# Kernel tuning notes

Hardware: AMD Instinct MI355X
Metric: run time of the kernel (lower is better)

## Reference

```python
import jax, jax.numpy as jnp
import numpy as np

B, H, W, C, NH = 400, 14, 14, 768, 12
HD = C // NH  # 64


def setup_inputs() -> dict:
    key = jax.random.key(0)
    ks = jax.random.split(key, 6)
    s = 0.02
    return {
        "hidden_states": jax.random.normal(ks[0], (B, H, W, C), jnp.float32),
        "qkv_w": jax.random.normal(ks[1], (3 * C, C), jnp.float32) * s,
        "qkv_b": jnp.zeros((3 * C,), jnp.float32),
        "proj_w": jax.random.normal(ks[2], (C, C), jnp.float32) * s,
        "proj_b": jnp.zeros((C,), jnp.float32),
        "rel_pos_h": jax.random.normal(ks[3], (2 * H - 1, HD), jnp.float32) * s,
        "rel_pos_w": jax.random.normal(ks[4], (2 * W - 1, HD), jnp.float32) * s,
    }


def _get_rel_pos(q_size, k_size, rel_pos):
    # q_size == k_size and table already has 2*k-1 entries -> pure gather,
    # matching SamVisionAttention.get_rel_pos without interpolation.
    coords = jnp.arange(q_size)[:, None] - jnp.arange(k_size)[None, :] + (k_size - 1)
    return rel_pos[coords]  # (q, k, head_dim)


def reference(hidden_states, qkv_w, qkv_b, proj_w, proj_b, rel_pos_h, rel_pos_w):
    b, h, w, c = hidden_states.shape
    scale = HD ** -0.5
    # qkv projection: (b, h*w, 3c) -> (3, b, nh, hw, hd)
    qkv = hidden_states.reshape(b, h * w, c) @ qkv_w.T + qkv_b
    qkv = qkv.reshape(b, h * w, 3, NH, HD).transpose(2, 0, 3, 1, 4)
    q, k, v = qkv[0], qkv[1], qkv[2]
    # decomposed relative position bias (computed from UNSCALED q, as in SAM)
    Rh = _get_rel_pos(h, h, rel_pos_h)  # (h, h, hd)
    Rw = _get_rel_pos(w, w, rel_pos_w)  # (w, w, hd)
    qr = q.reshape(b, NH, h, w, HD)
    rel_h = jnp.einsum('bnhwc,hkc->bnhwk', qr, Rh)  # (b, nh, h, w, h)
    rel_w = jnp.einsum('bnhwc,wkc->bnhwk', qr, Rw)  # (b, nh, h, w, w)
    bias = (rel_h[..., :, None] + rel_w[..., None, :]).reshape(b, NH, h * w, h * w)
    # attention
    attn = jnp.einsum('bnqd,bnkd->bnqk', q, k) * scale + bias
    attn = jax.nn.softmax(attn, axis=-1)
    out = jnp.einsum('bnqk,bnkd->bnqd', attn, v)
    out = out.transpose(0, 2, 1, 3).reshape(b, h, w, c)
    return out @ proj_w.T + proj_b
```

## Files before the change

### kernel.cpp

```cpp
#include <hip/hip_runtime.h>
#include <hip/hip_bf16.h>

typedef __bf16 bfv8 __attribute__((ext_vector_type(8)));
typedef float f32x4 __attribute__((ext_vector_type(4)));
typedef unsigned short u16;
typedef unsigned int u32;

#define MT 78400

#define SBAR() __builtin_amdgcn_s_barrier()
#define VMCNT(n) asm volatile("s_waitcnt vmcnt(" #n ")" ::: "memory")

__device__ __forceinline__ u16 f2bf(float f) {
  u32 x = __float_as_uint(f);
  return (u16)((x + 0x7FFFu + ((x >> 16) & 1u)) >> 16);
}

__device__ __forceinline__ void gld16(const void* g, void* l) {
  __builtin_amdgcn_global_load_lds((const __attribute__((address_space(1))) void*)g,
                                   (__attribute__((address_space(3))) void*)l, 16, 0, 0);
}

__global__ __launch_bounds__(256) void cvt_f32_bf16(const float* __restrict__ src,
                                                    u16* __restrict__ dst, int n8) {
  int stride = gridDim.x * 256;
  for (int i = blockIdx.x * 256 + threadIdx.x; i < n8; i += stride) {
    const float4* s = (const float4*)(src + (long)i * 8);
    float4 a = s[0], b = s[1];
    u32 p0 = f2bf(a.x) | ((u32)f2bf(a.y) << 16);
    u32 p1 = f2bf(a.z) | ((u32)f2bf(a.w) << 16);
    u32 p2 = f2bf(b.x) | ((u32)f2bf(b.y) << 16);
    u32 p3 = f2bf(b.z) | ((u32)f2bf(b.w) << 16);
    uint4 o = {p0, p1, p2, p3};
    *(uint4*)(dst + (long)i * 8) = o;
  }
}


__device__ __forceinline__ void stageA(const u16* __restrict__ A, u16* SH, int sl,
                                       int m0, int kt, int h, int tid) {
#pragma unroll
  for (int i = 0; i < 2; ++i) {
    int c = tid + 512 * i;
    int r = c >> 3, s = c & 7;
    int gc = s ^ (r & 7);
    int mr = m0 + h * 128 + r; if (mr > MT - 1) mr = MT - 1;
    gld16(A + mr * 768 + kt * 64 + gc * 8, SH + sl * 32768 + h * 8192 + c * 8);
  }
}

__device__ __forceinline__ void stageB(const u16* __restrict__ W, u16* SH, int sl,
                                       int n0, int kt, int h, int tid) {
#pragma unroll
  for (int i = 0; i < 2; ++i) {
    int c = tid + 512 * i;
    int r = c >> 3, s = c & 7;
    int gc = s ^ (r & 7);
    gld16(W + (n0 + h * 128 + r) * 768 + kt * 64 + gc * 8,
          SH + sl * 32768 + 16384 + h * 8192 + c * 8);
  }
}

__device__ __forceinline__ void gemm256_main(const u16* __restrict__ A, const u16* __restrict__ W,
                                             u16* SH, int m0, int n0, int tid,
                                             f32x4 (&acc)[8][4]) {
  const int lane = tid & 63;
  const int q15 = lane & 15, g = lane >> 4;
  const int wid = tid >> 6;
  const int wm = wid >> 2, wn = wid & 3;
  const int q7 = q15 & 7;
  const int x0 = (g ^ q7) << 3;
  const int arow0 = wm * 128 + q15;
  const int brow0 = wn * 64 + q15;

  stageB(W, SH, 0, n0, 0, 0, tid); stageB(W, SH, 0, n0, 0, 1, tid);
  stageA(A, SH, 0, m0, 0, 0, tid); stageA(A, SH, 0, m0, 0, 1, tid);
  stageB(W, SH, 1, n0, 1, 0, tid); stageB(W, SH, 1, n0, 1, 1, tid);
  VMCNT(4);
  SBAR();

  for (int u = 0; u < 12; ++u) {
    const int sl = u & 1;
    const u16* Sa = SH + sl * 32768;
    const u16* Sb = Sa + 16384;
    const int ka = (u + 1 < 12) ? u + 1 : 11;
    const int kb = (u + 2 < 12) ? u + 2 : 11;
    bfv8 b0[4], b1[4];
#pragma unroll
    for (int p = 0; p < 4; ++p) {
      if (p == 0) {
#pragma unroll
        for (int ni = 0; ni < 4; ++ni) {
          const u16* bp = Sb + (brow0 + ni * 16) * 64;
          b0[ni] = *(const bfv8*)(bp + x0);
          b1[ni] = *(const bfv8*)(bp + (x0 ^ 32));
        }
      }
      bfv8 a0[2], a1[2];
#pragma unroll
      for (int m2 = 0; m2 < 2; ++m2) {
        const u16* ap = Sa + (arow0 + (p * 2 + m2) * 16) * 64;
        a0[m2] = *(const bfv8*)(ap + x0);
        a1[m2] = *(const bfv8*)(ap + (x0 ^ 32));
      }
      if (p == 0)      stageA(A, SH, sl ^ 1, m0, ka, 0, tid);
      else if (p == 1) stageA(A, SH, sl ^ 1, m0, ka, 1, tid);
      else if (p == 2) stageB(W, SH, sl, n0, kb, 0, tid);
      else           { stageB(W, SH, sl, n0, kb, 1, tid); VMCNT(4); }
      SBAR();
      __builtin_amdgcn_s_setprio(1);
#pragma unroll
      for (int m2 = 0; m2 < 2; ++m2)
#pragma unroll
        for (int ni = 0; ni < 4; ++ni)
          acc[p * 2 + m2][ni] = __builtin_amdgcn_mfma_f32_16x16x32_bf16(a0[m2], b0[ni], acc[p * 2 + m2][ni], 0, 0, 0);
#pragma unroll
      for (int m2 = 0; m2 < 2; ++m2)
#pragma unroll
        for (int ni = 0; ni < 4; ++ni)
          acc[p * 2 + m2][ni] = __builtin_amdgcn_mfma_f32_16x16x32_bf16(a1[m2], b1[ni], acc[p * 2 + m2][ni], 0, 0, 0);
      __builtin_amdgcn_s_setprio(0);
      SBAR();
    }
  }
}

__global__ __launch_bounds__(512, 2) void qkv_gemm(const u16* __restrict__ A, const u16* __restrict__ W,
                                                   const float* __restrict__ bias,
                                                   u16* __restrict__ Qo, u16* __restrict__ Ko,
                                                   u16* __restrict__ Vo) {
  extern __shared__ u16 SH[];
  const int tid = threadIdx.x;
  const int orig = blockIdx.x;
  const int xcd = orig & 7, ii = orig >> 3;
  const int wg = (xcd < 3 ? xcd * 346 : 1038 + (xcd - 3) * 345) + ii;
  const int mt = wg / 9, nt = wg - mt * 9;
  const int m0 = mt * 256, n0 = nt * 256;

  f32x4 acc[8][4];
#pragma unroll
  for (int i = 0; i < 8; ++i)
#pragma unroll
    for (int j = 0; j < 4; ++j) acc[i][j] = (f32x4){0.f, 0.f, 0.f, 0.f};

  gemm256_main(A, W, SH, m0, n0, tid, acc);

  const int lane = tid & 63, q15 = lane & 15, g = lane >> 4;
  const int wid = tid >> 6, wm = wid >> 2, wn = wid & 3;
  __syncthreads();
  const int sel = nt / 3;
  u16* dst = (sel == 0) ? Qo : (sel == 1) ? Ko : Vo;
  const int ntr = nt - sel * 3;
  u16* Cs = SH;

#pragma unroll
  for (int h = 0; h < 2; ++h) {
    if (wm == h) {
#pragma unroll
      for (int ni = 0; ni < 4; ++ni) {
        int col = wn * 64 + ni * 16 + q15;
        float bb = bias[n0 + col];
#pragma unroll
        for (int mi = 0; mi < 8; ++mi)
#pragma unroll
          for (int r = 0; r < 4; ++r)
            Cs[(mi * 16 + g * 4 + r) * 264 + col] = f2bf(acc[mi][ni][r] + bb);
      }
    }
    __syncthreads();
#pragma unroll
    for (int j = 0; j < 8; ++j) {
      int idx = tid + 512 * j;
      int row = idx >> 5, cc = idx & 31;
      int m = m0 + h * 128 + row;
      if (m < MT) {
        int b = m / 196, s = m - b * 196;
        int nh = ntr * 4 + (cc >> 3);
        int hd0 = (cc & 7) * 8;
        uint4 v = *(const uint4*)(Cs + row * 264 + cc * 8);
        *(uint4*)(dst + (long)b * 150528 + (long)s * 64 + nh * 12544 + hd0) = v;
      }
    }
    if (h == 0) __syncthreads();
  }
}

__global__ __launch_bounds__(512, 2) void proj_gemm(const u16* __restrict__ A, const u16* __restrict__ W,
                                                    const float* __restrict__ bias,
                                                    float* __restrict__ out) {
  extern __shared__ u16 SH[];
  const int tid = threadIdx.x;
  const int orig = blockIdx.x;
  const int xcd = orig & 7, ii = orig >> 3;
  const int wg = (xcd < 1 ? xcd * 116 : 116 + (xcd - 1) * 115) + ii;
  const int mt = wg / 3, nt = wg - mt * 3;
  const int m0 = mt * 256, n0 = nt * 256;

  f32x4 acc[8][4];
#pragma unroll
  for (int i = 0; i < 8; ++i)
#pragma unroll
    for (int j = 0; j < 4; ++j) acc[i][j] = (f32x4){0.f, 0.f, 0.f, 0.f};

  gemm256_main(A, W, SH, m0, n0, tid, acc);

  const int lane = tid & 63, q15 = lane & 15, g = lane >> 4;
  const int wid = tid >> 6, wm = wid >> 2, wn = wid & 3;

#pragma unroll
  for (int ni = 0; ni < 4; ++ni) {
    int n = n0 + wn * 64 + ni * 16 + q15;
    float bb = bias[n];
#pragma unroll
    for (int mi = 0; mi < 8; ++mi)
#pragma unroll
      for (int r = 0; r < 4; ++r) {
        int m = m0 + wm * 128 + mi * 16 + g * 4 + r;
        if (m < MT) out[(long)m * 768 + n] = acc[mi][ni][r] + bb;
      }
  }
}

#define KLDS_OFF 0
#define INDK_OFF 29952
#define VT_OFF   46592
#define TH_OFF   79360
#define TW_OFF   83248
#define AW_OFF   87136
#define P_OFF    97376
#define SMEM_SZ  156768

__global__ __launch_bounds__(512, 2) void attn_kernel(const u16* __restrict__ Q, const u16* __restrict__ K,
                                                      const u16* __restrict__ V,
                                                      const float* __restrict__ rph, const float* __restrict__ rpw,
                                                      u16* __restrict__ AO) {
  extern __shared__ char smem[];
  u16* Klds = (u16*)(smem + KLDS_OFF);
  u16* IndK = (u16*)(smem + INDK_OFF);
  u16* VT = (u16*)(smem + VT_OFF);
  u16* TH = (u16*)(smem + TH_OFF);
  u16* TW = (u16*)(smem + TW_OFF);
  const int tid = threadIdx.x, lane = tid & 63, wid = tid >> 6;
  const int q15 = lane & 15, g = lane >> 4;
  const int bnh = blockIdx.x;
  const int b = bnh / 12, nh = bnh - b * 12;
  const u16* Qg = Q + bnh * 12544;
  const u16* Kg = K + bnh * 12544;
  const u16* Vg = V + bnh * 12544;
  u16* Pw = (u16*)(smem + P_OFF) + wid * 16 * 232;
  u16* AWw = (u16*)(smem + AW_OFF) + wid * 16 * 40;

  for (int c = tid; c < 1764; c += 512) {
    int krow = c / 9, part = c - krow * 9;
    gld16(Kg + krow * 64 + part * 8, Klds + c * 8);
  }
  for (int i = tid; i < 208 * 40; i += 512) {
    int k = i / 40, j = i - (i / 40) * 40;
    int hk = k / 14, wk = k - hk * 14;
    IndK[i] = (j == hk || j == 16 + wk) ? 0x3F80 : 0;
  }
  for (int idx = tid; idx < 1792; idx += 512) {
    int k = idx >> 3, nb = idx & 7;
    u32 w0 = 0, w1 = 0, w2 = 0, w3 = 0;
    if (k < 196) {
      uint4 t = *(const uint4*)(Vg + k * 64 + nb * 8);
      w0 = t.x; w1 = t.y; w2 = t.z; w3 = t.w;
    }
    u32 wv[4] = {w0, w1, w2, w3};
#pragma unroll
    for (int j = 0; j < 8; j++) {
      int n = nb * 8 + j;
      u16 val = (u16)(wv[j >> 1] >> ((j & 1) * 16));
      int blk = (k >> 3) ^ (n & 7) ^ (n >> 3);
      VT[n * 256 + blk * 8 + (k & 7)] = val;
    }
  }
  for (int i = tid; i < 27 * 64; i += 512) {
    int r = i >> 6, cc = i & 63;
    TH[r * 72 + cc] = f2bf(rph[i]);
    TW[r * 72 + cc] = f2bf(rpw[i]);
  }
  for (int i = lane; i < 16 * 24; i += 64) Pw[(i / 24) * 232 + 208 + (i % 24)] = 0;
  __syncthreads();

  const f32x4 zero = {0.f, 0.f, 0.f, 0.f};
  for (int qt = wid; qt < 13; qt += 8) {
    const int q0 = qt * 16;
    int qrow = q0 + q15; if (qrow > 195) qrow = 195;
    bfv8 qf0 = *(const bfv8*)(Qg + qrow * 64 + g * 8);
    bfv8 qf1 = *(const bfv8*)(Qg + qrow * 64 + 32 + g * 8);

    int hq0 = q0 / 14, hq1 = (q0 + 15) / 14;
    int rha = hq0 + 13 - q15; rha = rha < 0 ? 0 : (rha > 26 ? 26 : rha);
    int rhb = hq1 + 13 - q15; rhb = rhb < 0 ? 0 : (rhb > 26 ? 26 : rhb);
    int rwa = q15;
    int rwb = 16 + q15; if (rwb > 26) rwb = 26;
    f32x4 c0h = zero, c1h = zero, c0w = zero, c1w = zero;
    {
      bfv8 t0 = *(const bfv8*)(TH + rha * 72 + g * 8);
      bfv8 t1 = *(const bfv8*)(TH + rha * 72 + 32 + g * 8);
      c0h = __builtin_amdgcn_mfma_f32_16x16x32_bf16(qf0, t0, c0h, 0, 0, 0);
      c0h = __builtin_amdgcn_mfma_f32_16x16x32_bf16(qf1, t1, c0h, 0, 0, 0);
      bfv8 t2 = *(const bfv8*)(TH + rhb * 72 + g * 8);
      bfv8 t3 = *(const bfv8*)(TH + rhb * 72 + 32 + g * 8);
      c1h = __builtin_amdgcn_mfma_f32_16x16x32_bf16(qf0, t2, c1h, 0, 0, 0);
      c1h = __builtin_amdgcn_mfma_f32_16x16x32_bf16(qf1, t3, c1h, 0, 0, 0);
      bfv8 u0 = *(const bfv8*)(TW + rwa * 72 + g * 8);
      bfv8 u1 = *(const bfv8*)(TW + rwa * 72 + 32 + g * 8);
      c0w = __builtin_amdgcn_mfma_f32_16x16x32_bf16(qf0, u0, c0w, 0, 0, 0);
      c0w = __builtin_amdgcn_mfma_f32_16x16x32_bf16(qf1, u1, c0w, 0, 0, 0);
      bfv8 u2 = *(const bfv8*)(TW + rwb * 72 + g * 8);
      bfv8 u3 = *(const bfv8*)(TW + rwb * 72 + 32 + g * 8);
      c1w = __builtin_amdgcn_mfma_f32_16x16x32_bf16(qf0, u2, c1w, 0, 0, 0);
      c1w = __builtin_amdgcn_mfma_f32_16x16x32_bf16(qf1, u3, c1w, 0, 0, 0);
    }

#pragma unroll
    for (int r = 0; r < 4; r++) {
      int row = g * 4 + r;
      int qq = q0 + row;
      int hqr = qq / 14;
      int wq_r = qq - hqr * 14;
      if (q15 < 10) AWw[row * 40 + 30 + q15] = 0;
      float rh = ((hqr == hq1) ? c1h[r] : c0h[r]) * 8.0f;
      AWw[row * 40 + q15] = (q15 <= 13) ? f2bf(rh) : (u16)0;
      int w0p = wq_r + 13 - q15;
      if (w0p >= 0 && w0p <= 13) AWw[row * 40 + 16 + w0p] = f2bf(c0w[r] * 8.0f);
      int w1p = wq_r - 3 - q15;
      if (w1p >= 0 && w1p <= 13) AWw[row * 40 + 16 + w1p] = f2bf(c1w[r] * 8.0f);
    }
    bfv8 qaug = *(const bfv8*)(AWw + q15 * 40 + g * 8);

    float den[4] = {0.f, 0.f, 0.f, 0.f};
#pragma unroll
    for (int t = 0; t < 13; t++) {
      bfv8 kb0 = *(const bfv8*)(Klds + (t * 16 + q15) * 72 + g * 8);
      bfv8 kb1 = *(const bfv8*)(Klds + (t * 16 + q15) * 72 + 32 + g * 8);
      bfv8 ib = *(const bfv8*)(IndK + (t * 16 + q15) * 40 + g * 8);
      __builtin_amdgcn_s_setprio(1);
      f32x4 a0 = __builtin_amdgcn_mfma_f32_16x16x32_bf16(qaug, ib, zero, 0, 0, 0);
      f32x4 a1 = __builtin_amdgcn_mfma_f32_16x16x32_bf16(qf0, kb0, a0, 0, 0, 0);
      f32x4 st = __builtin_amdgcn_mfma_f32_16x16x32_bf16(qf1, kb1, a1, 0, 0, 0);
      __builtin_amdgcn_s_setprio(0);
#pragma unroll
      for (int r = 0; r < 4; r++) {
        float v = st[r] * 0.125f - 4.0f;
        float p = (t == 12 && q15 >= 4) ? 0.f : exp2f(v * 1.44269504f);
        den[r] += p;
        Pw[(g * 4 + r) * 232 + t * 16 + q15] = f2bf(p);
      }
    }
#pragma unroll
    for (int r = 0; r < 4; r++) {
      den[r] += __shfl_xor(den[r], 1);
      den[r] += __shfl_xor(den[r], 2);
      den[r] += __shfl_xor(den[r], 4);
      den[r] += __shfl_xor(den[r], 8);
    }

    f32x4 o[4] = {zero, zero, zero, zero};
    __builtin_amdgcn_s_setprio(1);
#pragma unroll
    for (int ks = 0; ks < 7; ks++) {
      bfv8 pa = *(const bfv8*)(Pw + q15 * 232 + ks * 32 + g * 8);
#pragma unroll
      for (int nt = 0; nt < 4; nt++) {
        int n = nt * 16 + q15;
        int blk = ((ks * 4 + g) ^ (n & 7) ^ (n >> 3));
        bfv8 vb = *(const bfv8*)(VT + n * 256 + blk * 8);
        o[nt] = __builtin_amdgcn_mfma_f32_16x16x32_bf16(pa, vb, o[nt], 0, 0, 0);
      }
    }
    __builtin_amdgcn_s_setprio(0);

    float inv[4];
#pragma unroll
    for (int r = 0; r < 4; r++) inv[r] = 1.0f / den[r];
#pragma unroll
    for (int nt = 0; nt < 4; nt++)
#pragma unroll
      for (int r = 0; r < 4; r++) {
        int s_ = q0 + g * 4 + r;
        if (s_ < 196) AO[((long)(b * 196 + s_)) * 768 + nh * 64 + nt * 16 + q15] = f2bf(o[nt][r] * inv[r]);
      }
  }
}

#define GEMM_LDS 131072

extern "C" void kernel_launch(void* const* d_in, const int* in_sizes, int n_in,
                              void* d_out, int out_size, void* d_ws, size_t ws_size,
                              hipStream_t stream) {
  const float* hs = (const float*)d_in[0];
  const float* qkvw = (const float*)d_in[1];
  const float* qkvb = (const float*)d_in[2];
  const float* projw = (const float*)d_in[3];
  const float* projb = (const float*)d_in[4];
  const float* rph = (const float*)d_in[5];
  const float* rpw = (const float*)d_in[6];

  char* ws = (char*)d_ws;
  u16* Xb = (u16*)ws;
  u16* Wq = (u16*)(ws + 120422400);
  u16* Wp = (u16*)(ws + 123961344);
  u16* Qb = (u16*)(ws + 125140992);
  u16* Kb = (u16*)(ws + 245563392);
  u16* Vb = (u16*)(ws + 365985792);
  u16* AO = Xb;

  cvt_f32_bf16<<<2048, 256, 0, stream>>>(hs, Xb, 7526400);
  cvt_f32_bf16<<<864, 256, 0, stream>>>(qkvw, Wq, 221184);
  cvt_f32_bf16<<<288, 256, 0, stream>>>(projw, Wp, 73728);

  hipFuncSetAttribute((const void*)qkv_gemm, hipFuncAttributeMaxDynamicSharedMemorySize, GEMM_LDS);
  qkv_gemm<<<2763, 512, GEMM_LDS, stream>>>(Xb, Wq, qkvb, Qb, Kb, Vb);

  hipFuncSetAttribute((const void*)attn_kernel, hipFuncAttributeMaxDynamicSharedMemorySize, SMEM_SZ);
  attn_kernel<<<4800, 512, SMEM_SZ, stream>>>(Qb, Kb, Vb, rph, rpw, AO);

  hipFuncSetAttribute((const void*)proj_gemm, hipFuncAttributeMaxDynamicSharedMemorySize, GEMM_LDS);
  proj_gemm<<<921, 512, GEMM_LDS, stream>>>(AO, Wp, projb, (float*)d_out);
}
```

Before: 866.8 us.

## Software-pipeline GEMM LDS fragment loads and swizzle K tile in attention

Restructures the GEMM main loop so the A/B fragment reads for the next sub-step are issued from LDS right after a barrier and overlap the MFMAs of the current step. The B fragments and first A fragments for the next k-tile are prefetched at the end of each iteration, and the staging order is rearranged to match. In the attention kernel, the padded K tile in LDS (stride 72) is replaced with an XOR-swizzled stride-64 layout, which shrinks shared memory and avoids bank conflicts. The scale and log2e constants in the softmax exponent are folded into one fused multiply-add. The new schedule adds register pressure and depends on the reordered barriers and vmcnt waits being correct.

```diff
diff --git a/kernel.cpp b/kernel.cpp
--- a/kernel.cpp
+++ b/kernel.cpp
@@ -68,61 +68,137 @@
   const int q15 = lane & 15, g = lane >> 4;
   const int wid = tid >> 6;
   const int wm = wid >> 2, wn = wid & 3;
-  const int q7 = q15 & 7;
-  const int x0 = (g ^ q7) << 3;
+  const int x0 = (g ^ (q15 & 7)) << 3;
   const int arow0 = wm * 128 + q15;
   const int brow0 = wn * 64 + q15;
+
+  bfv8 b0[4], b1[4];
+  bfv8 aX0[2], aX1[2], aY0[2], aY1[2];
 
   stageB(W, SH, 0, n0, 0, 0, tid); stageB(W, SH, 0, n0, 0, 1, tid);
   stageA(A, SH, 0, m0, 0, 0, tid); stageA(A, SH, 0, m0, 0, 1, tid);
   stageB(W, SH, 1, n0, 1, 0, tid); stageB(W, SH, 1, n0, 1, 1, tid);
+  stageA(A, SH, 1, m0, 1, 0, tid);
   VMCNT(4);
   SBAR();
+  {
+    const u16* Sb = SH + 16384;
+#pragma unroll
+    for (int ni = 0; ni < 4; ++ni) {
+      const u16* bp = Sb + (brow0 + ni * 16) * 64;
+      b0[ni] = *(const bfv8*)(bp + x0);
+      b1[ni] = *(const bfv8*)(bp + (x0 ^ 32));
+    }
+#pragma unroll
+    for (int m2 = 0; m2 < 2; ++m2) {
+      const u16* ap = SH + (arow0 + m2 * 16) * 64;
+      aX0[m2] = *(const bfv8*)(ap + x0);
+      aX1[m2] = *(const bfv8*)(ap + (x0 ^ 32));
+    }
+  }
 
   for (int u = 0; u < 12; ++u) {
     const int sl = u & 1;
     const u16* Sa = SH + sl * 32768;
-    const u16* Sb = Sa + 16384;
-    const int ka = (u + 1 < 12) ? u + 1 : 11;
-    const int kb = (u + 2 < 12) ? u + 2 : 11;
-    bfv8 b0[4], b1[4];
-#pragma unroll
-    for (int p = 0; p < 4; ++p) {
-      if (p == 0) {
-#pragma unroll
-        for (int ni = 0; ni < 4; ++ni) {
-          const u16* bp = Sb + (brow0 + ni * 16) * 64;
-          b0[ni] = *(const bfv8*)(bp + x0);
-          b1[ni] = *(const bfv8*)(bp + (x0 ^ 32));
-        }
-      }
-      bfv8 a0[2], a1[2];
+    const u16* San = SH + (sl ^ 1) * 32768;
+    const u16* Sbn = San + 16384;
+    const int kn1 = (u + 1 < 12) ? u + 1 : 11;
+    const int kn2 = (u + 2 < 12) ? u + 2 : 11;
+
+    __builtin_amdgcn_s_setprio(1);
+#pragma unroll
+    for (int m2 = 0; m2 < 2; ++m2)
+#pragma unroll
+      for (int ni = 0; ni < 4; ++ni)
+        acc[m2][ni] = __builtin_amdgcn_mfma_f32_16x16x32_bf16(aX0[m2], b0[ni], acc[m2][ni], 0, 0, 0);
+#pragma unroll
+    for (int m2 = 0; m2 < 2; ++m2)
+#pragma unroll
+      for (int ni = 0; ni < 4; ++ni)
+        acc[m2][ni] = __builtin_amdgcn_mfma_f32_16x16x32_bf16(aX1[m2], b1[ni], acc[m2][ni], 0, 0, 0);
+    __builtin_amdgcn_s_setprio(0);
+    SBAR();
+#pragma unroll
+    for (int m2 = 0; m2 < 2; ++m2) {
+      const u16* ap = Sa + (arow0 + (2 + m2) * 16) * 64;
+      aY0[m2] = *(const bfv8*)(ap + x0);
+      aY1[m2] = *(const bfv8*)(ap + (x0 ^ 32));
+    }
+    stageA(A, SH, sl ^ 1, m0, kn1, 1, tid);
+
+    __builtin_amdgcn_s_setprio(1);
+#pragma unroll
+    for (int m2 = 0; m2 < 2; ++m2)
+#pragma unroll
+      for (int ni = 0; ni < 4; ++ni)
+        acc[2 + m2][ni] = __builtin_amdgcn_mfma_f32_16x16x32_bf16(aY0[m2], b0[ni], acc[2 + m2][ni], 0, 0, 0);
+#pragma unroll
+    for (int m2 = 0; m2 < 2; ++m2)
+#pragma unroll
+      for (int ni = 0; ni < 4; ++ni)
+        acc[2 + m2][ni] = __builtin_amdgcn_mfma_f32_16x16x32_bf16(aY1[m2], b1[ni], acc[2 + m2][ni], 0, 0, 0);
+    __builtin_amdgcn_s_setprio(0);
+    SBAR();
+#pragma unroll
+    for (int m2 = 0; m2 < 2; ++m2) {
+      const u16* ap = Sa + (arow0 + (4 + m2) * 16) * 64;
+      aX0[m2] = *(const bfv8*)(ap + x0);
+      aX1[m2] = *(const bfv8*)(ap + (x0 ^ 32));
+    }
+    stageB(W, SH, sl, n0, kn2, 0, tid);
+
+    __builtin_amdgcn_s_setprio(1);
+#pragma unroll
+    for (int m2 = 0; m2 < 2; ++m2)
+#pragma unroll
+      for (int ni = 0; ni < 4; ++ni)
+        acc[4 + m2][ni] = __builtin_amdgcn_mfma_f32_16x16x32_bf16(aX0[m2], b0[ni], acc[4 + m2][ni], 0, 0, 0);
+#pragma unroll
+    for (int m2 = 0; m2 < 2; ++m2)
+#pragma unroll
+      for (int ni = 0; ni < 4; ++ni)
+        acc[4 + m2][ni] = __builtin_amdgcn_mfma_f32_16x16x32_bf16(aX1[m2], b1[ni], acc[4 + m2][ni], 0, 0, 0);
+    __builtin_amdgcn_s_setprio(0);
+    SBAR();
+#pragma unroll
+    for (int m2 = 0; m2 < 2; ++m2) {
+      const u16* ap = Sa + (arow0 + (6 + m2) * 16) * 64;
+      aY0[m2] = *(const bfv8*)(ap + x0);
+      aY1[m2] = *(const bfv8*)(ap + (x0 ^ 32));
+    }
+    stageB(W, SH, sl, n0, kn2, 1, tid);
+
+    __builtin_amdgcn_s_setprio(1);
+#pragma unroll
+    for (int m2 = 0; m2 < 2; ++m2)
+#pragma unroll
+      for (int ni = 0; ni < 4; ++ni)
+        acc[6 + m2][ni] = __builtin_amdgcn_mfma_f32_16x16x32_bf16(aY0[m2], b0[ni], acc[6 + m2][ni], 0, 0, 0);
+#pragma unroll
+    for (int m2 = 0; m2 < 2; ++m2)
+#pragma unroll
+      for (int ni = 0; ni < 4; ++ni)
+        acc[6 + m2][ni] = __builtin_amdgcn_mfma_f32_16x16x32_bf16(aY1[m2], b1[ni], acc[6 + m2][ni], 0, 0, 0);
+    __builtin_amdgcn_s_setprio(0);
+    VMCNT(4);
+    SBAR();
+    if (u < 11) {
+#pragma unroll
+      for (int ni = 0; ni < 4; ++ni) {
+        const u16* bp = Sbn + (brow0 + ni * 16) * 64;
+        b0[ni] = *(const bfv8*)(bp + x0);
+        b1[ni] = *(const bfv8*)(bp + (x0 ^ 32));
+      }
 #pragma unroll
       for (int m2 = 0; m2 < 2; ++m2) {
-        const u16* ap = Sa + (arow0 + (p * 2 + m2) * 16) * 64;
-        a0[m2] = *(const bfv8*)(ap + x0);
-        a1[m2] = *(const bfv8*)(ap + (x0 ^ 32));
-      }
-      if (p == 0)      stageA(A, SH, sl ^ 1, m0, ka, 0, tid);
-      else if (p == 1) stageA(A, SH, sl ^ 1, m0, ka, 1, tid);
-      else if (p == 2) stageB(W, SH, sl, n0, kb, 0, tid);
-      else           { stageB(W, SH, sl, n0, kb, 1, tid); VMCNT(4); }
-      SBAR();
-      __builtin_amdgcn_s_setprio(1);
-#pragma unroll
-      for (int m2 = 0; m2 < 2; ++m2)
-#pragma unroll
-        for (int ni = 0; ni < 4; ++ni)
-          acc[p * 2 + m2][ni] = __builtin_amdgcn_mfma_f32_16x16x32_bf16(a0[m2], b0[ni], acc[p * 2 + m2][ni], 0, 0, 0);
-#pragma unroll
-      for (int m2 = 0; m2 < 2; ++m2)
-#pragma unroll
-        for (int ni = 0; ni < 4; ++ni)
-          acc[p * 2 + m2][ni] = __builtin_amdgcn_mfma_f32_16x16x32_bf16(a1[m2], b1[ni], acc[p * 2 + m2][ni], 0, 0, 0);
-      __builtin_amdgcn_s_setprio(0);
-      SBAR();
-    }
-  }
+        const u16* ap = San + (arow0 + m2 * 16) * 64;
+        aX0[m2] = *(const bfv8*)(ap + x0);
+        aX1[m2] = *(const bfv8*)(ap + (x0 ^ 32));
+      }
+    }
+    stageA(A, SH, sl, m0, kn2, 0, tid);
+  }
+  VMCNT(0);
 }
 
 __global__ __launch_bounds__(512, 2) void qkv_gemm(const u16* __restrict__ A, const u16* __restrict__ W,
@@ -222,13 +298,13 @@
 }
 
 #define KLDS_OFF 0
-#define INDK_OFF 29952
-#define VT_OFF   46592
-#define TH_OFF   79360
-#define TW_OFF   83248
-#define AW_OFF   87136
-#define P_OFF    97376
-#define SMEM_SZ  156768
+#define INDK_OFF 26624
+#define VT_OFF   43264
+#define TH_OFF   76032
+#define TW_OFF   79920
+#define AW_OFF   83808
+#define P_OFF    94048
+#define SMEM_SZ  153440
 
 __global__ __launch_bounds__(512, 2) void attn_kernel(const u16* __restrict__ Q, const u16* __restrict__ K,
                                                       const u16* __restrict__ V,
@@ -250,9 +326,9 @@
   u16* Pw = (u16*)(smem + P_OFF) + wid * 16 * 232;
   u16* AWw = (u16*)(smem + AW_OFF) + wid * 16 * 40;
 
-  for (int c = tid; c < 1764; c += 512) {
-    int krow = c / 9, part = c - krow * 9;
-    gld16(Kg + krow * 64 + part * 8, Klds + c * 8);
+  for (int c = tid; c < 1568; c += 512) {
+    int krow = c >> 3, part = c & 7;
+    gld16(Kg + krow * 64 + ((part ^ (krow & 7)) << 3), Klds + c * 8);
   }
   for (int i = tid; i < 208 * 40; i += 512) {
     int k = i / 40, j = i - (i / 40) * 40;
@@ -282,6 +358,10 @@
   }
   for (int i = lane; i < 16 * 24; i += 64) Pw[(i / 24) * 232 + 208 + (i % 24)] = 0;
   __syncthreads();
+
+  const int ksw = q15 & 7;
+  const int ko0 = (g ^ ksw) << 3;
+  const int ko1 = ((g + 4) ^ ksw) << 3;
 
   const f32x4 zero = {0.f, 0.f, 0.f, 0.f};
   for (int qt = wid; qt < 13; qt += 8) {
@@ -334,8 +414,9 @@
     float den[4] = {0.f, 0.f, 0.f, 0.f};
 #pragma unroll
     for (int t = 0; t < 13; t++) {
-      bfv8 kb0 = *(const bfv8*)(Klds + (t * 16 + q15) * 72 + g * 8);
-      bfv8 kb1 = *(const bfv8*)(Klds + (t * 16 + q15) * 72 + 32 + g * 8);
+      const u16* kr = Klds + (t * 16 + q15) * 64;
+      bfv8 kb0 = *(const bfv8*)(kr + ko0);
+      bfv8 kb1 = *(const bfv8*)(kr + ko1);
       bfv8 ib = *(const bfv8*)(IndK + (t * 16 + q15) * 40 + g * 8);
       __builtin_amdgcn_s_setprio(1);
       f32x4 a0 = __builtin_amdgcn_mfma_f32_16x16x32_bf16(qaug, ib, zero, 0, 0, 0);
@@ -344,8 +425,7 @@
       __builtin_amdgcn_s_setprio(0);
 #pragma unroll
       for (int r = 0; r < 4; r++) {
-        float v = st[r] * 0.125f - 4.0f;
-        float p = (t == 12 && q15 >= 4) ? 0.f : exp2f(v * 1.44269504f);
+        float p = (t == 12 && q15 >= 4) ? 0.f : exp2f(st[r] * 0.18033688f - 5.7707802f);
         den[r] += p;
         Pw[(g * 4 + r) * 232 + t * 16 + q15] = f2bf(p);
       }
```

After: 845.5 us. 1.03x faster.
